# Optimization experiments

Hardware: AMD Instinct MI355X
Metric: run time of the kernel (lower is better)

## Reference

```python
import jax, jax.numpy as jnp
import numpy as np

# module constants (from init_kwargs)
OUT_W = 22
OUT_H = 48
IN_H = 64
IN_W = 44
DT_OFF = 0.5
DX_OFF = 0.5
DY_OFF = 0.5
SIGMA_OFF = 1.0
DELTA_T_OFF = 1.0
DELTA_OFF = 1.0
EPS = 1e-8
ATT_H = int(round(OUT_W / IN_W * IN_H))  # 32

N, C, T, H, W = 16, 64, 30, 64, 44


def setup_inputs() -> dict:
    key = jax.random.key(0)
    ks = jax.random.split(key, 8)
    inp = {"x": jax.random.normal(ks[0], (N, C, T, H, W), dtype=jnp.float32)}
    names = ["dt", "dx", "dy", "log_sigma2", "log_delta_t", "log_delta", "log_gamma"]
    for i, nm in enumerate(names):
        inp[nm] = jax.random.normal(ks[i + 1], (N, 1), dtype=jnp.float32)
    return inp


def _filterbank(mu, grid_len, sigma2):
    # mu: [N, out_len]; sigma2: [N,1,1] -> F: [N, out_len, grid_len], row-normalized
    g = jnp.arange(grid_len, dtype=jnp.float32)  # [grid_len]
    F = jnp.exp(-((g[None, None, :] - mu[:, :, None]) ** 2) / (2.0 * sigma2))
    return F / jnp.maximum(F.sum(axis=2, keepdims=True), EPS)


def reference(x, dt, dx, dy, log_sigma2, log_delta_t, log_delta, log_gamma):
    n, c, t, h, w = x.shape
    anchor_t, anchor_x, anchor_y = t * DT_OFF, w * DX_OFF, h * DY_OFF

    dt_ = jnp.tanh(dt) * t / 2.0 + anchor_t          # [N,1]
    dx_ = jnp.tanh(dx) * IN_W / 2.0 + anchor_x
    dy_ = jnp.tanh(dy) * IN_H / 2.0 + anchor_y
    sigma2 = (jnp.exp(log_sigma2) * SIGMA_OFF).reshape(-1, 1, 1)
    delta_t = jnp.exp(log_delta_t) * DELTA_T_OFF
    delta = jnp.exp(log_delta) * DELTA_OFF
    gamma = jax.nn.sigmoid(log_gamma)

    gt = jnp.arange(t, dtype=jnp.float32)[None, :]
    gx = jnp.arange(OUT_W, dtype=jnp.float32)[None, :]
    gy = jnp.arange(ATT_H, dtype=jnp.float32)[None, :]
    mu_t = dt_ + (gt - t / 2.0) * delta_t            # [N,T]
    mu_x = dx_ + (gx - OUT_W / 2.0) * delta          # [N,out_w]
    mu_y = dy_ + (gy - ATT_H / 2.0) * delta          # [N,att_h]

    Ft = _filterbank(mu_t, t, sigma2)                # [N,T,T]
    Fx = _filterbank(mu_x, w, sigma2)                # [N,out_w,W]
    Fy = _filterbank(mu_y, h, sigma2)                # [N,att_h,H]

    # glimpse = Ft @ (Fy @ x @ Fx^T) over appropriate axes
    g = jnp.einsum('ncthw,naw->nctha', x, Fx)        # [N,C,T,H,out_w]
    g = jnp.einsum('nctha,nbh->nctba', g, Fy)        # [N,C,T,att_h,out_w]
    g = jnp.einsum('nctba,nst->ncsba', g, Ft)        # [N,C,T,att_h,out_w]

    out = g * gamma.reshape(-1, 1, 1, 1, 1)
    pad_t = (OUT_H - ATT_H) // 2
    pad_b = OUT_H - pad_t - ATT_H
    out = jnp.pad(out, ((0, 0), (0, 0), (0, 0), (pad_t, pad_b), (0, 0)))
    return out
```

## Files before the change

### kernel.cpp

```cpp
#include <hip/hip_runtime.h>
#include <hip/hip_fp16.h>

#define XN 16
#define XC 64
#define XT 30
#define XH 64
#define XW 44
#define OUTW 22
#define ATTH 32
#define OUTH 48
#define SLICE (XH*XW)
#define OSLICE (OUTH*OUTW)

#define WS_FX 0
#define WS_FY (3*64*4)
#define WS_FT (WS_FY + 4*64*4)
#define WS_N  (WS_FT + 2*64*4)

typedef _Float16 f16;
typedef f16 f16x8 __attribute__((ext_vector_type(8)));
typedef float f32x16 __attribute__((ext_vector_type(16)));
typedef float f32x4 __attribute__((ext_vector_type(4)));

__device__ __forceinline__ unsigned int PK(float a, float b) {
    return __builtin_bit_cast(unsigned int, __builtin_amdgcn_cvt_pkrtz(a, b));
}
__device__ __forceinline__ f32x16 MF(uint4 a, uint4 b, f32x16 c) {
    return __builtin_amdgcn_mfma_f32_32x32x16_f16(
        __builtin_bit_cast(f16x8, a), __builtin_bit_cast(f16x8, b), c, 0, 0, 0);
}
__device__ __forceinline__ f32x16 ZF() {
    f32x16 z;
    #pragma unroll
    for (int i = 0; i < 16; ++i) z[i] = 0.f;
    return z;
}

__global__ void prep_kernel(const float* __restrict__ dtp, const float* __restrict__ dxp,
                            const float* __restrict__ dyp, const float* __restrict__ ls2,
                            const float* __restrict__ ldt, const float* __restrict__ ldp,
                            unsigned int* __restrict__ ws)
{
    __shared__ float fx[22][44];
    __shared__ float fy[32][64];
    __shared__ float ft[30][32];
    const int n = blockIdx.x;
    const int r = threadIdx.x;
    const float dt_ = tanhf(dtp[n]) * 15.f + 15.f;
    const float dx_ = tanhf(dxp[n]) * 22.f + 22.f;
    const float dy_ = tanhf(dyp[n]) * 32.f + 32.f;
    const float inv2s = 1.f / (2.f * expf(ls2[n]));
    const float delta_t = expf(ldt[n]);
    const float delta = expf(ldp[n]);

    if (r < 30) {
        float mu = dt_ + (float)(r - 15) * delta_t;
        float e[30]; float sum = 0.f;
        for (int t = 0; t < 30; ++t) { float d = (float)t - mu; float v = expf(-d*d*inv2s); e[t] = v; sum += v; }
        float inv = 1.f / fmaxf(sum, 1e-8f);
        for (int t = 0; t < 30; ++t) ft[r][t] = e[t] * inv;
        ft[r][30] = 0.f; ft[r][31] = 0.f;
    } else if (r < 52) {
        int a = r - 30;
        float mu = dx_ + (float)(a - 11) * delta;
        float e[44]; float sum = 0.f;
        for (int w = 0; w < 44; ++w) { float d = (float)w - mu; float v = expf(-d*d*inv2s); e[w] = v; sum += v; }
        float inv = 1.f / fmaxf(sum, 1e-8f);
        for (int w = 0; w < 44; ++w) fx[a][w] = e[w] * inv;
    } else if (r < 84) {
        int b = r - 52;
        float mu = dy_ + (float)(b - 16) * delta;
        float e[64]; float sum = 0.f;
        for (int h = 0; h < 64; ++h) { float d = (float)h - mu; float v = expf(-d*d*inv2s); e[h] = v; sum += v; }
        float inv = 1.f / fmaxf(sum, 1e-8f);
        for (int h = 0; h < 64; ++h) fy[b][h] = e[h] * inv;
    }
    __syncthreads();

    if (r < 64) {
        const int al = r & 31, hf = r >> 5;
        unsigned int* wn = ws + n * WS_N;
        #pragma unroll
        for (int kt = 0; kt < 3; ++kt) {
            int w0 = kt*16 + 8*hf;
            float v[8];
            #pragma unroll
            for (int i = 0; i < 8; ++i) { int w = w0 + i; v[i] = (al < 22 && w < 44) ? fx[al][w] : 0.f; }
            #pragma unroll
            for (int j = 0; j < 4; ++j) {
                unsigned int lo = __half_as_ushort(__float2half_rn(v[2*j]));
                unsigned int hi = __half_as_ushort(__float2half_rn(v[2*j+1]));
                wn[WS_FX + (kt*64 + r)*4 + j] = lo | (hi << 16);
            }
        }
        #pragma unroll
        for (int kt = 0; kt < 4; ++kt) {
            int h0 = kt*16 + 8*hf;
            float v[8];
            #pragma unroll
            for (int i = 0; i < 8; ++i) v[i] = fy[al][h0 + i];
            #pragma unroll
            for (int j = 0; j < 4; ++j) {
                unsigned int lo = __half_as_ushort(__float2half_rn(v[2*j]));
                unsigned int hi = __half_as_ushort(__float2half_rn(v[2*j+1]));
                wn[WS_FY + (kt*64 + r)*4 + j] = lo | (hi << 16);
            }
        }
        #pragma unroll
        for (int kt = 0; kt < 2; ++kt) {
            int t0 = kt*16 + 8*hf;
            float v[8];
            #pragma unroll
            for (int i = 0; i < 8; ++i) v[i] = (al < 30) ? ft[al][t0 + i] : 0.f;
            #pragma unroll
            for (int j = 0; j < 4; ++j) {
                unsigned int lo = __half_as_ushort(__float2half_rn(v[2*j]));
                unsigned int hi = __half_as_ushort(__float2half_rn(v[2*j+1]));
                wn[WS_FT + (kt*64 + r)*4 + j] = lo | (hi << 16);
            }
        }
    }
}

__global__ __launch_bounds__(256, 2) void glimpse_kernel(
    const float* __restrict__ x, const unsigned int* __restrict__ ws,
    const float* __restrict__ p_lg, float* __restrict__ out)
{
    const int tid = threadIdx.x;
    const int n = blockIdx.x >> 6, c = blockIdx.x & 63;
    const int wv = tid >> 6, l = tid & 63;
    const int al = l & 31, hf = l >> 5;

    __shared__ unsigned int a1t[4][32*34];
    __shared__ unsigned int a2t[704*17];

    for (int r = tid; r < 704; r += 256) { a2t[r*17 + 15] = 0u; a2t[r*17 + 16] = 0u; }

    const size_t obase = (size_t)(n*XC + c) * (XT*OSLICE);
    {
        f32x4 z4 = {0.f, 0.f, 0.f, 0.f};
        f32x4* out4 = (f32x4*)(out + obase);
        #pragma unroll
        for (int k2 = 0; k2 < 11; ++k2) {
            int idx = tid + k2*256;
            if (idx < 2640) {
                int s = idx / 88;
                int rr = idx - s*88;
                int j = (rr < 44) ? rr : (rr + 176);
                __builtin_nontemporal_store(z4, out4 + s*264 + j);
            }
        }
    }

    const unsigned int* wn = ws + n * WS_N;
    uint4 fxf[3], fyf[4], ftf[2];
    #pragma unroll
    for (int kt = 0; kt < 3; ++kt) fxf[kt] = *(const uint4*)(wn + WS_FX + (kt*64 + l)*4);
    #pragma unroll
    for (int kt = 0; kt < 4; ++kt) fyf[kt] = *(const uint4*)(wn + WS_FY + (kt*64 + l)*4);
    #pragma unroll
    for (int kt = 0; kt < 2; ++kt) ftf[kt] = *(const uint4*)(wn + WS_FT + (kt*64 + l)*4);

    const float gamma = 1.f / (1.f + expf(-p_lg[n]));

    unsigned int* myA1 = &a1t[wv][0];
    unsigned short* a2t16 = (unsigned short*)a2t;
    const float* xc = x + (size_t)(n*XC + c) * (XT*SLICE);

    #pragma unroll 2
    for (int t = wv; t < XT; t += 4) {
        const float* xs = xc + (size_t)t * SLICE;
        f32x16 D0 = ZF(), D1m = ZF(), D2 = ZF();
        #pragma unroll
        for (int mt = 0; mt < 2; ++mt) {
            const float* rb = xs + (mt*32 + al)*44;
            float4 A0 = *(const float4*)(rb + 8*hf);
            float4 A1v = *(const float4*)(rb + 8*hf + 4);
            float4 B0 = *(const float4*)(rb + 16 + 8*hf);
            float4 B1 = *(const float4*)(rb + 16 + 8*hf + 4);
            float4 C0 = *(const float4*)(rb + 32 + 8*hf);
            float4 C1 = (hf == 0) ? *(const float4*)(rb + 36) : make_float4(0.f,0.f,0.f,0.f);
            uint4 u0 = make_uint4(PK(A0.x,A0.y), PK(A0.z,A0.w), PK(A1v.x,A1v.y), PK(A1v.z,A1v.w));
            uint4 u1 = make_uint4(PK(B0.x,B0.y), PK(B0.z,B0.w), PK(B1.x,B1.y), PK(B1.z,B1.w));
            uint4 u2 = make_uint4(PK(C0.x,C0.y), PK(C0.z,C0.w), PK(C1.x,C1.y), PK(C1.z,C1.w));
            if (mt == 0) {
                D0 = MF(u0, fxf[0], D0); D0 = MF(u1, fxf[1], D0); D0 = MF(u2, fxf[2], D0);
            } else {
                D1m = MF(u0, fxf[0], D1m); D1m = MF(u1, fxf[1], D1m); D1m = MF(u2, fxf[2], D1m);
            }
        }
        #pragma unroll
        for (int j = 0; j < 8; ++j) {
            int wofs = (j & 1) + 4*(j >> 1) + 2*hf;
            myA1[al*34 + wofs]      = PK(D0[2*j],  D0[2*j+1]);
            myA1[al*34 + wofs + 16] = PK(D1m[2*j], D1m[2*j+1]);
        }
        #pragma unroll
        for (int kt = 0; kt < 4; ++kt) {
            int base = al*34 + kt*8 + 4*hf;
            uint4 bw;
            bw.x = myA1[base]; bw.y = myA1[base+1]; bw.z = myA1[base+2]; bw.w = myA1[base+3];
            D2 = MF(fyf[kt], bw, D2);
        }
        if (al < 22) {
            #pragma unroll
            for (int q = 0; q < 16; ++q) {
                int b = (q & 3) + 8*(q >> 2) + 4*hf;
                unsigned short hv = __builtin_bit_cast(unsigned short, (_Float16)D2[q]);
                a2t16[(b*22 + al)*34 + t] = hv;
            }
        }
    }
    __syncthreads();

    #pragma unroll 2
    for (int nt = wv; nt < 22; nt += 4) {
        int ba = nt*32 + al;
        f32x16 D3 = ZF();
        #pragma unroll
        for (int kt = 0; kt < 2; ++kt) {
            int base = ba*17 + kt*8 + 4*hf;
            uint4 bw;
            bw.x = a2t[base]; bw.y = a2t[base+1]; bw.z = a2t[base+2]; bw.w = a2t[base+3];
            D3 = MF(ftf[kt], bw, D3);
        }
        float* ob = out + obase + 176 + ba;
        #pragma unroll
        for (int q = 0; q < 16; ++q) {
            int s = (q & 3) + 8*(q >> 2) + 4*hf;
            if (s < XT) __builtin_nontemporal_store(gamma * D3[q], ob + s*OSLICE);
        }
    }
}

extern "C" void kernel_launch(void* const* d_in, const int* in_sizes, int n_in,
                              void* d_out, int out_size, void* d_ws, size_t ws_size,
                              hipStream_t stream) {
    const float* x   = (const float*)d_in[0];
    const float* dt  = (const float*)d_in[1];
    const float* dx  = (const float*)d_in[2];
    const float* dy  = (const float*)d_in[3];
    const float* ls2 = (const float*)d_in[4];
    const float* ldt = (const float*)d_in[5];
    const float* ld  = (const float*)d_in[6];
    const float* lg  = (const float*)d_in[7];
    float* out = (float*)d_out;
    unsigned int* ws = (unsigned int*)d_ws;

    prep_kernel<<<dim3(XN), dim3(96), 0, stream>>>(dt, dx, dy, ls2, ldt, ld, ws);
    glimpse_kernel<<<dim3(XN * XC), dim3(256), 0, stream>>>(x, ws, lg, out);
}
```

Baseline: 112.7 us.

## Replace LDS staging of first GEMM result with cross-lane shuffles

Removes the per-wave a1t shared-memory buffer that held the Fx-contracted tile between the first and second MFMA stages. Lanes now exchange packed fp16 halves with __shfl_xor across the 32-lane halves to build the B fragment directly in registers. The x loads for both row tiles are hoisted to the top of the loop, the loop unroll drops from 2 to 1, and launch bounds are raised to 3 blocks per CU. The goal is to cut LDS traffic and LDS footprint so more blocks fit, at the cost of register pressure and less cross-iteration overlap.

New measurement: 116.5 us. 1.03x slower.

```diff
diff --git a/kernel.cpp b/kernel.cpp
--- a/kernel.cpp
+++ b/kernel.cpp
@@ -122,7 +122,7 @@
     }
 }
 
-__global__ __launch_bounds__(256, 2) void glimpse_kernel(
+__global__ __launch_bounds__(256, 3) void glimpse_kernel(
     const float* __restrict__ x, const unsigned int* __restrict__ ws,
     const float* __restrict__ p_lg, float* __restrict__ out)
 {
@@ -131,7 +131,6 @@
     const int wv = tid >> 6, l = tid & 63;
     const int al = l & 31, hf = l >> 5;
 
-    __shared__ unsigned int a1t[4][32*34];
     __shared__ unsigned int a2t[704*17];
 
     for (int r = tid; r < 704; r += 256) { a2t[r*17 + 15] = 0u; a2t[r*17 + 16] = 0u; }
@@ -163,45 +162,68 @@
 
     const float gamma = 1.f / (1.f + expf(-p_lg[n]));
 
-    unsigned int* myA1 = &a1t[wv][0];
     unsigned short* a2t16 = (unsigned short*)a2t;
     const float* xc = x + (size_t)(n*XC + c) * (XT*SLICE);
 
-    #pragma unroll 2
+    #pragma unroll 1
     for (int t = wv; t < XT; t += 4) {
         const float* xs = xc + (size_t)t * SLICE;
+        const float* rb0 = xs + al*44;
+        const float* rb1 = xs + (32 + al)*44;
+        float4 A0a = *(const float4*)(rb0 + 8*hf);
+        float4 A1a = *(const float4*)(rb0 + 8*hf + 4);
+        float4 B0a = *(const float4*)(rb0 + 16 + 8*hf);
+        float4 B1a = *(const float4*)(rb0 + 16 + 8*hf + 4);
+        float4 C0a = *(const float4*)(rb0 + 32 + 8*hf);
+        float4 C1a = (hf == 0) ? *(const float4*)(rb0 + 36) : make_float4(0.f,0.f,0.f,0.f);
+        float4 A0b = *(const float4*)(rb1 + 8*hf);
+        float4 A1b = *(const float4*)(rb1 + 8*hf + 4);
+        float4 B0b = *(const float4*)(rb1 + 16 + 8*hf);
+        float4 B1b = *(const float4*)(rb1 + 16 + 8*hf + 4);
+        float4 C0b = *(const float4*)(rb1 + 32 + 8*hf);
+        float4 C1b = (hf == 0) ? *(const float4*)(rb1 + 36) : make_float4(0.f,0.f,0.f,0.f);
+
         f32x16 D0 = ZF(), D1m = ZF(), D2 = ZF();
-        #pragma unroll
-        for (int mt = 0; mt < 2; ++mt) {
-            const float* rb = xs + (mt*32 + al)*44;
-            float4 A0 = *(const float4*)(rb + 8*hf);
-            float4 A1v = *(const float4*)(rb + 8*hf + 4);
-            float4 B0 = *(const float4*)(rb + 16 + 8*hf);
-            float4 B1 = *(const float4*)(rb + 16 + 8*hf + 4);
-            float4 C0 = *(const float4*)(rb + 32 + 8*hf);
-            float4 C1 = (hf == 0) ? *(const float4*)(rb + 36) : make_float4(0.f,0.f,0.f,0.f);
-            uint4 u0 = make_uint4(PK(A0.x,A0.y), PK(A0.z,A0.w), PK(A1v.x,A1v.y), PK(A1v.z,A1v.w));
-            uint4 u1 = make_uint4(PK(B0.x,B0.y), PK(B0.z,B0.w), PK(B1.x,B1.y), PK(B1.z,B1.w));
-            uint4 u2 = make_uint4(PK(C0.x,C0.y), PK(C0.z,C0.w), PK(C1.x,C1.y), PK(C1.z,C1.w));
-            if (mt == 0) {
-                D0 = MF(u0, fxf[0], D0); D0 = MF(u1, fxf[1], D0); D0 = MF(u2, fxf[2], D0);
-            } else {
-                D1m = MF(u0, fxf[0], D1m); D1m = MF(u1, fxf[1], D1m); D1m = MF(u2, fxf[2], D1m);
-            }
-        }
-        #pragma unroll
-        for (int j = 0; j < 8; ++j) {
-            int wofs = (j & 1) + 4*(j >> 1) + 2*hf;
-            myA1[al*34 + wofs]      = PK(D0[2*j],  D0[2*j+1]);
-            myA1[al*34 + wofs + 16] = PK(D1m[2*j], D1m[2*j+1]);
-        }
-        #pragma unroll
-        for (int kt = 0; kt < 4; ++kt) {
-            int base = al*34 + kt*8 + 4*hf;
-            uint4 bw;
-            bw.x = myA1[base]; bw.y = myA1[base+1]; bw.z = myA1[base+2]; bw.w = myA1[base+3];
-            D2 = MF(fyf[kt], bw, D2);
-        }
+        {
+            uint4 u0 = make_uint4(PK(A0a.x,A0a.y), PK(A0a.z,A0a.w), PK(A1a.x,A1a.y), PK(A1a.z,A1a.w));
+            uint4 u1 = make_uint4(PK(B0a.x,B0a.y), PK(B0a.z,B0a.w), PK(B1a.x,B1a.y), PK(B1a.z,B1a.w));
+            uint4 u2 = make_uint4(PK(C0a.x,C0a.y), PK(C0a.z,C0a.w), PK(C1a.x,C1a.y), PK(C1a.z,C1a.w));
+            D0 = MF(u0, fxf[0], D0); D0 = MF(u1, fxf[1], D0); D0 = MF(u2, fxf[2], D0);
+        }
+        {
+            uint4 u0 = make_uint4(PK(A0b.x,A0b.y), PK(A0b.z,A0b.w), PK(A1b.x,A1b.y), PK(A1b.z,A1b.w));
+            uint4 u1 = make_uint4(PK(B0b.x,B0b.y), PK(B0b.z,B0b.w), PK(B1b.x,B1b.y), PK(B1b.z,B1b.w));
+            uint4 u2 = make_uint4(PK(C0b.x,C0b.y), PK(C0b.z,C0b.w), PK(C1b.x,C1b.y), PK(C1b.z,C1b.w));
+            D1m = MF(u0, fxf[0], D1m); D1m = MF(u1, fxf[1], D1m); D1m = MF(u2, fxf[2], D1m);
+        }
+
+        #pragma unroll
+        for (int half = 0; half < 2; ++half) {
+            const f32x16& D = half ? D1m : D0;
+            unsigned int w0g[4], w1g[4];
+            #pragma unroll
+            for (int g = 0; g < 4; ++g) {
+                w0g[g] = PK(D[4*g],   D[4*g+1]);
+                w1g[g] = PK(D[4*g+2], D[4*g+3]);
+            }
+            #pragma unroll
+            for (int ktl = 0; ktl < 2; ++ktl) {
+                const int gA = 2*ktl, gB = 2*ktl + 1;
+                unsigned int own0 = hf ? w0g[gB] : w0g[gA];
+                unsigned int own1 = hf ? w1g[gB] : w1g[gA];
+                unsigned int snd0 = hf ? w0g[gA] : w0g[gB];
+                unsigned int snd1 = hf ? w1g[gA] : w1g[gB];
+                unsigned int rcv0 = (unsigned int)__shfl_xor((int)snd0, 32, 64);
+                unsigned int rcv1 = (unsigned int)__shfl_xor((int)snd1, 32, 64);
+                uint4 frag;
+                frag.x = hf ? rcv0 : own0;
+                frag.y = hf ? rcv1 : own1;
+                frag.z = hf ? own0 : rcv0;
+                frag.w = hf ? own1 : rcv1;
+                D2 = MF(fyf[half*2 + ktl], frag, D2);
+            }
+        }
+
         if (al < 22) {
             #pragma unroll
             for (int q = 0; q < 16; ++q) {
```
